# Performance work log

Measured on AMD Instinct MI355X. Metric: run time of the kernel, lower is better.

Reference implementation:

```python
import jax, jax.numpy as jnp
import numpy as np

B, H, W, C = 8, 64, 64, 128
L = H * W
NH = 4
HD = C // NH
SCALE = HD ** -0.5
WIN = 8
SHIFT = 4
DEPTH = 2
K = 3
N = WIN * WIN
NW = (H // WIN) * (W // WIN)


def _rel_pos_index(win):
    coords = np.stack(np.meshgrid(np.arange(win), np.arange(win), indexing='ij'))
    cf = coords.reshape(2, -1)
    rel = (cf[:, :, None] - cf[:, None, :]).transpose(1, 2, 0).copy()
    rel[:, :, 0] += win - 1
    rel[:, :, 1] += win - 1
    rel[:, :, 0] *= 2 * win - 1
    return rel.sum(-1)  # (N, N)

REL_IDX = jnp.asarray(_rel_pos_index(WIN).reshape(-1))


def _attn_mask(Hh, Ww, win, shift):
    img = np.zeros((Hh, Ww))
    cnt = 0
    for hs in (slice(0, -win), slice(-win, -shift), slice(-shift, None)):
        for ws in (slice(0, -win), slice(-win, -shift), slice(-shift, None)):
            img[hs, ws] = cnt
            cnt += 1
    mw = img.reshape(Hh // win, win, Ww // win, win).transpose(0, 2, 1, 3).reshape(-1, win * win)
    m = mw[:, None, :] - mw[:, :, None]
    return jnp.asarray(np.where(m != 0, -100.0, 0.0).astype(np.float32))  # (nW, N, N)

ATTN_MASK = _attn_mask(H, W, WIN, SHIFT)


def layer_norm(x, g, b, eps=1e-5):
    mu = x.mean(-1, keepdims=True)
    var = x.var(-1, keepdims=True)
    return (x - mu) / jnp.sqrt(var + eps) * g + b


def window_partition(x, win):
    Bb, Hh, Ww, Cc = x.shape
    x = x.reshape(Bb, Hh // win, win, Ww // win, win, Cc)
    return x.transpose(0, 1, 3, 2, 4, 5).reshape(-1, win, win, Cc)


def window_reverse(wins, win, Hh, Ww):
    Bb = wins.shape[0] // (Hh * Ww // win // win)
    x = wins.reshape(Bb, Hh // win, Ww // win, win, win, -1)
    return x.transpose(0, 1, 3, 2, 4, 5).reshape(Bb, Hh, Ww, -1)


def swin_block(x, shift, n1g, n1b, qkvw, qkvb, rp, pw, pb, n2g, n2b, f1w, f1b, f2w, f2b):
    shortcut = x
    x = layer_norm(x, n1g, n1b).reshape(B, H, W, C)
    if shift > 0:
        x = jnp.roll(x, (-shift, -shift), axis=(1, 2))
    xw = window_partition(x, WIN).reshape(-1, N, C)  # (B*nW, N, C)
    qkv = (xw @ qkvw + qkvb).reshape(-1, N, 3, NH, HD).transpose(2, 0, 3, 1, 4)
    q, k, v = qkv[0] * SCALE, qkv[1], qkv[2]
    attn = jnp.einsum('whnd,whmd->whnm', q, k)  # (B*nW, NH, N, N)
    bias = rp[REL_IDX].reshape(N, N, NH).transpose(2, 0, 1)
    attn = attn + bias[None]
    if shift > 0:
        attn = (attn.reshape(B, NW, NH, N, N) + ATTN_MASK[None, :, None]).reshape(-1, NH, N, N)
    attn = jax.nn.softmax(attn, axis=-1)
    out = jnp.einsum('whnm,whmd->whnd', attn, v).transpose(0, 2, 1, 3).reshape(-1, N, C)
    out = out @ pw + pb
    x = window_reverse(out.reshape(-1, WIN, WIN, C), WIN, H, W)
    if shift > 0:
        x = jnp.roll(x, (shift, shift), axis=(1, 2))
    x = shortcut + x.reshape(B, L, C)
    h = layer_norm(x, n2g, n2b)
    h = jax.nn.gelu(h @ f1w + f1b, approximate=False) @ f2w + f2b
    return x + h


def conv1d(x, w, b):  # x (B,C,L), w (O,I,K)
    y = jax.lax.conv_general_dilated(x, w, (1,), [(K // 2, K // 2)], dimension_numbers=('NCH', 'OIH', 'NCH'))
    return y + b[None, :, None]


def deform_conv1d(xt, off_w, off_b, msk_w, msk_b):
    x = xt.transpose(0, 2, 1)  # (B, C, L)
    offset = conv1d(x, off_w, off_b)                    # (B, K, L)
    mask = jax.nn.sigmoid(conv1d(x, msk_w, msk_b))      # (B, K, L)
    i = jnp.arange(L, dtype=x.dtype)
    pos = jnp.clip(i[None, None, :] + offset, 0.0, L - 1)  # (B, K, L)
    fp = jnp.floor(pos).astype(jnp.int32)
    cp = jnp.minimum(fp + 1, L - 1)
    alpha = pos - fp.astype(x.dtype)
    idx_f = jnp.broadcast_to(fp[:, None], (B, C, K, L))
    idx_c = jnp.broadcast_to(cp[:, None], (B, C, K, L))
    xe = jnp.broadcast_to(x[:, :, None, :], (B, C, K, L))
    xf = jnp.take_along_axis(xe, idx_f, axis=3)
    xc = jnp.take_along_axis(xe, idx_c, axis=3)
    samp = xf * (1.0 - alpha[:, None]) + xc * alpha[:, None]
    out = (samp * mask[:, None]).sum(2)  # (B, C, L)
    # faithful to torch: output.view(B, L, out_channels) reinterprets memory, no transpose
    return out.reshape(B, L, C)


def _forward(xt, hx, cx, red_w, red_b, n1g, n1b, qkvw, qkvb, rp, pw, pb, n2g, n2b,
             f1w, f1b, f2w, f2b, off_w, off_b, msk_w, msk_b, lf_w, lf_b, gf_w, gf_b, ff_w, ff_b):
    # global branch: inject hidden state then W-MSA / SW-MSA blocks
    g = jnp.concatenate([xt, hx], axis=-1) @ red_w + red_b
    for i, shift in enumerate((0, SHIFT)):
        g = swin_block(g, shift, n1g[i], n1b[i], qkvw[i], qkvb[i], rp[i], pw[i], pb[i],
                       n2g[i], n2b[i], f1w[i], f1b[i], f2w[i], f2b[i])
    # local branch: deformable 1D conv over token axis
    local = deform_conv1d(xt, off_w, off_b, msk_w, msk_b)
    # local-global fusion
    fu = jax.nn.relu((local @ lf_w + lf_b) * (g @ gf_w + gf_b)) @ ff_w + ff_b
    # LSTM-style gating (SwinLSTM cell update)
    gate = jax.nn.sigmoid(fu)
    cell = jnp.tanh(fu)
    cy = gate * (cx + cell)
    hy = gate * jnp.tanh(cy)
    return hy


def setup_inputs():
    key = jax.random.key(0)
    ks = iter(jax.random.split(key, 24))
    def rn(shape, s=0.02):
        return jax.random.normal(next(ks), shape, jnp.float32) * s
    return dict(
        xt=jax.random.normal(next(ks), (B, L, C), jnp.float32),
        hx=jax.random.normal(next(ks), (B, L, C), jnp.float32),
        cx=jax.random.normal(next(ks), (B, L, C), jnp.float32),
        red_w=rn((2 * C, C)), red_b=jnp.zeros((C,), jnp.float32),
        n1g=jnp.ones((DEPTH, C), jnp.float32), n1b=jnp.zeros((DEPTH, C), jnp.float32),
        qkvw=rn((DEPTH, C, 3 * C)), qkvb=jnp.zeros((DEPTH, 3 * C), jnp.float32),
        rp=rn((DEPTH, (2 * WIN - 1) ** 2, NH)),
        pw=rn((DEPTH, C, C)), pb=jnp.zeros((DEPTH, C), jnp.float32),
        n2g=jnp.ones((DEPTH, C), jnp.float32), n2b=jnp.zeros((DEPTH, C), jnp.float32),
        f1w=rn((DEPTH, C, 4 * C)), f1b=jnp.zeros((DEPTH, 4 * C), jnp.float32),
        f2w=rn((DEPTH, 4 * C, C)), f2b=jnp.zeros((DEPTH, C), jnp.float32),
        off_w=rn((K, C, K)), off_b=jnp.zeros((K,), jnp.float32),
        msk_w=rn((K, C, K)), msk_b=jnp.zeros((K,), jnp.float32),
        lf_w=rn((C, C)), lf_b=jnp.zeros((C,), jnp.float32),
        gf_w=rn((C, C)), gf_b=jnp.zeros((C,), jnp.float32),
        ff_w=rn((C, C)), ff_b=jnp.zeros((C,), jnp.float32),
    )


def reference(xt, hx, cx, red_w, red_b, n1g, n1b, qkvw, qkvb, rp, pw, pb, n2g, n2b,
              f1w, f1b, f2w, f2b, off_w, off_b, msk_w, msk_b, lf_w, lf_b, gf_w, gf_b, ff_w, ff_b):
    return _forward(xt, hx, cx, red_w, red_b, n1g, n1b, qkvw, qkvb, rp, pw, pb, n2g, n2b,
                    f1w, f1b, f2w, f2b, off_w, off_b, msk_w, msk_b, lf_w, lf_b, gf_w, gf_b, ff_w, ff_b)
```

## Files before the change

kernel.cpp:

```cpp
#include <hip/hip_runtime.h>
#include <hip/hip_bf16.h>
#include <math.h>

typedef __hip_bfloat16 bf16;
typedef unsigned short u16;
#define BF(x) __bfloat162float(x)
static __device__ __forceinline__ bf16 FB(float x) { return __float2bfloat16(x); }
static __device__ __forceinline__ u16 FBu(float x) {
    bf16 b = __float2bfloat16(x);
    return *(u16*)&b;
}

typedef __attribute__((ext_vector_type(4))) float f32x4;
typedef __attribute__((ext_vector_type(8))) __bf16 bf16x8;


#define O_REDW 0
#define O_QKVW 32768
#define O_PW   131072
#define O_F1W  163840
#define O_F2W  294912
#define O_LFW  425984
#define O_GFW  442368
#define O_FFW  458752
#define O_REDB 475136
#define O_QKVB 475264
#define O_PB   476032
#define O_F1B  476288
#define O_F2B  477312
#define O_LFB  477568
#define O_GFB  477696
#define O_FFB  477824
#define O_RP   477952
#define O_N1G  479752
#define O_N1B  480008
#define O_N2G  480264
#define O_N2B  480520
#define O_OW   480776
#define O_OB   481928
#define O_MW   481931
#define O_MB   483083

#define ROW_S 36
#define CH_S  2320

__device__ __forceinline__ int get_mode(const void* xt) {
    const unsigned* w = (const unsigned*)xt;
    int zlo = 0, inband = 0;
    #pragma unroll
    for (int i = 0; i < 32; ++i) {
        unsigned lo = w[i] & 0xFFFFu;
        int e = (int)((lo >> 7) & 0xFF);
        zlo += (lo == 0u || lo == 0x8000u);
        inband += (e >= 100 && e <= 140);
    }
    if (zlo >= 29) return 1;
    return (inband >= 20) ? 0 : 1;
}

__device__ __forceinline__ float LD(const void* p, size_t i, int mode) {
    return mode ? ((const float*)p)[i] : BF(((const bf16*)p)[i]);
}

__device__ __forceinline__ void async16(const u16* g, u16* l) {
    __builtin_amdgcn_global_load_lds(
        (const __attribute__((address_space(1))) unsigned int*)g,
        (__attribute__((address_space(3))) unsigned int*)l, 16, 0, 0);
}

struct PrepT { const void* src; int srcOff, K, N, dstOff; };
struct Prep { PrepT d[29]; int start[30]; };

__global__ void prep_k(Prep p, bf16* __restrict__ dst, const void* __restrict__ dtp) {
    const int mode = get_mode(dtp);
    int i = blockIdx.x * 256 + threadIdx.x;
    if (i >= p.start[29]) return;
    int s = 0;
    while (p.start[s + 1] <= i) ++s;
    int e = i - p.start[s];
    float v;
    if (p.d[s].N > 0) {
        int n = e / p.d[s].K, k = e % p.d[s].K;
        v = LD(p.d[s].src, (size_t)p.d[s].srcOff + (size_t)k * p.d[s].N + n, mode);
    } else {
        v = LD(p.d[s].src, (size_t)p.d[s].srcOff + e, mode);
    }
    dst[p.d[s].dstOff + e] = FB(v);
}

__launch_bounds__(256)
__global__ void xcat_k(const void* __restrict__ xt, const void* __restrict__ hx,
                       u16* __restrict__ X) {
    const int mode = get_mode(xt);
    const int total = 32768 * 32;
    for (int gidx = blockIdx.x * 256 + threadIdx.x; gidx < total;
         gidx += gridDim.x * 256) {
        int r = gidx >> 5, gi = gidx & 31;
        const void* src = (gi < 16) ? xt : hx;
        int c = (gi & 15) << 3;
        u16 outv[8];
        if (mode) {
            const float* s = (const float*)src + (size_t)r * 128 + c;
            float4 a = *(const float4*)s;
            float4 b = *(const float4*)(s + 4);
            outv[0] = FBu(a.x); outv[1] = FBu(a.y); outv[2] = FBu(a.z); outv[3] = FBu(a.w);
            outv[4] = FBu(b.x); outv[5] = FBu(b.y); outv[6] = FBu(b.z); outv[7] = FBu(b.w);
        } else {
            *(uint4*)outv = *(const uint4*)((const u16*)src + (size_t)r * 128 + c);
        }
        *(uint4*)(X + (size_t)r * 256 + (gi << 3)) = *(const uint4*)outv;
    }
}

template <int EPI>
__launch_bounds__(256)
__global__ void gemm_mfma(const u16* __restrict__ A, const u16* __restrict__ Bt,
                          const bf16* __restrict__ bias, bf16* __restrict__ outb,
                          float* __restrict__ outf, int M, int N, int K, int shift) {
    __shared__ __align__(16) u16 Als[2][2048];
    __shared__ __align__(16) u16 Bls[2][4096];
    const int tid = threadIdx.x;
    const int wave = tid >> 6, lane = tid & 63;
    const int q = lane >> 4, lr = lane & 15;
    const int wm = (wave >> 1) << 5, wn = (wave & 1) << 6;
    const int bm = blockIdx.y << 6, bn = blockIdx.x << 7;
    const f32x4 zero = {0.f, 0.f, 0.f, 0.f};
    f32x4 acc[2][4];
    #pragma unroll
    for (int i = 0; i < 2; ++i)
        #pragma unroll
        for (int j = 0; j < 4; ++j) acc[i][j] = zero;

    const int nk = K >> 5;
    {
        int c = tid;
        async16(A + (size_t)(bm + (c >> 2)) * K + ((c & 3) << 3), Als[0] + (c << 3));
        #pragma unroll
        for (int c2 = tid; c2 < 512; c2 += 256)
            async16(Bt + (size_t)(bn + (c2 >> 2)) * K + ((c2 & 3) << 3), Bls[0] + (c2 << 3));
    }
    __syncthreads();

    for (int i = 0; i < nk; ++i) {
        const int cur = i & 1, nxt = cur ^ 1;
        if (i + 1 < nk) {
            int k1 = (i + 1) << 5;
            int c = tid;
            async16(A + (size_t)(bm + (c >> 2)) * K + k1 + ((c & 3) << 3), Als[nxt] + (c << 3));
            #pragma unroll
            for (int c2 = tid; c2 < 512; c2 += 256)
                async16(Bt + (size_t)(bn + (c2 >> 2)) * K + k1 + ((c2 & 3) << 3), Bls[nxt] + (c2 << 3));
        }
        bf16x8 af[2], bfr[4];
        #pragma unroll
        for (int t = 0; t < 2; ++t)
            af[t] = *(const bf16x8*)(Als[cur] + ((wm + (t << 4) + lr) << 5) + (q << 3));
        #pragma unroll
        for (int t = 0; t < 4; ++t)
            bfr[t] = *(const bf16x8*)(Bls[cur] + ((wn + (t << 4) + lr) << 5) + (q << 3));
        #pragma unroll
        for (int mt = 0; mt < 2; ++mt)
            #pragma unroll
            for (int nt = 0; nt < 4; ++nt)
                acc[mt][nt] = __builtin_amdgcn_mfma_f32_16x16x32_bf16(
                    af[mt], bfr[nt], acc[mt][nt], 0, 0, 0);
        __syncthreads();
    }

    #pragma unroll
    for (int nt = 0; nt < 4; ++nt) {
        int col = bn + wn + (nt << 4) + lr;
        float bv = BF(bias[col]);
        #pragma unroll
        for (int mt = 0; mt < 2; ++mt) {
            int row0 = bm + wm + (mt << 4) + (q << 2);
            #pragma unroll
            for (int i = 0; i < 4; ++i) {
                int r = row0 + i;
                float v = acc[mt][nt][i] + bv;
                size_t idx = (size_t)r * N + col;
                if (EPI == 0) {
                    outb[idx] = FB(v);
                } else if (EPI == 3) {
                    int b = r >> 12, rem = r & 4095;
                    int wi = rem >> 6, n = rem & 63;
                    int hp = ((wi >> 3) << 3) + (n >> 3);
                    int wp = ((wi & 7) << 3) + (n & 7);
                    int h = (hp + shift) & 63, w = (wp + shift) & 63;
                    outf[((size_t)((b << 12) + (h << 6) + w)) * 128 + col] += v;
                } else if (EPI == 5) {
                    outf[idx] = v;
                }
            }
        }
    }
}

__launch_bounds__(256)
__global__ void qkvln_k(const float* __restrict__ g, const u16* __restrict__ wtu,
                        const bf16* __restrict__ wtb, u16* __restrict__ qkv,
                        int d, int shift) {
    __shared__ __align__(16) u16 Ach[4 * CH_S];
    __shared__ __align__(16) u16 Bb[2][8192];
    const int tid = threadIdx.x;
    const int wave = tid >> 6, lane = tid & 63;
    const int q = lane >> 4, lr = lane & 15;
    const int wm = (wave >> 1) << 5, wn = (wave & 1) << 6;
    const int bm = blockIdx.x << 6;
    const u16* Wq = wtu + O_QKVW + d * 49152;

    #pragma unroll
    for (int i = tid; i < 1024; i += 256) {
        int kc = i >> 9, c = i & 511;
        async16(Wq + (size_t)(c >> 2) * 128 + (kc << 5) + ((c & 3) << 3),
                Bb[0] + (kc << 12) + (c << 3));
    }

    {
        int row = tid >> 2, qtr = tid & 3;
        int r = bm + row;
        int b = r >> 12, rem = r & 4095;
        int wi = rem >> 6, n = rem & 63;
        int hp = ((wi >> 3) << 3) + (n >> 3);
        int wp = ((wi & 7) << 3) + (n & 7);
        int h = (hp + shift) & 63, w = (wp + shift) & 63;
        int src = (b << 12) + (h << 6) + w;
        const float* gr = g + (size_t)src * 128 + qtr * 32;
        float vals[32];
        float s1 = 0.f, s2 = 0.f;
        #pragma unroll
        for (int i = 0; i < 8; ++i) {
            float4 v4 = *(const float4*)(gr + i * 4);
            vals[i * 4] = v4.x; vals[i * 4 + 1] = v4.y;
            vals[i * 4 + 2] = v4.z; vals[i * 4 + 3] = v4.w;
            s1 += v4.x + v4.y + v4.z + v4.w;
            s2 += v4.x * v4.x + v4.y * v4.y + v4.z * v4.z + v4.w * v4.w;
        }
        s1 += __shfl_xor(s1, 1); s1 += __shfl_xor(s1, 2);
        s2 += __shfl_xor(s2, 1); s2 += __shfl_xor(s2, 2);
        float mu = s1 * (1.f / 128.f);
        float var = s2 * (1.f / 128.f) - mu * mu;
        float inv = rsqrtf(var + 1e-5f);
        #pragma unroll
        for (int i = 0; i < 32; ++i) {
            int c = qtr * 32 + i;
            float o = (vals[i] - mu) * inv * BF(wtb[O_N1G + d * 128 + c])
                      + BF(wtb[O_N1B + d * 128 + c]);
            Ach[qtr * CH_S + row * ROW_S + i] = FBu(o);
        }
    }
    __syncthreads();

    const f32x4 zero = {0.f, 0.f, 0.f, 0.f};
    f32x4 acc[2][4];
    for (int s = 0; s < 6; ++s) {
        const int nc = s >> 1, kh = s & 1, cur = s & 1 ? (s & 1) : (s & 1);
        const int bsel = s & 1;
        if (s < 5) {
            int t = s + 1, nct = t >> 1, kht = t & 1;
            const u16* Bg = Wq + nct * 16384;
            #pragma unroll
            for (int i = tid; i < 1024; i += 256) {
                int kc = i >> 9, c = i & 511;
                async16(Bg + (size_t)(c >> 2) * 128 + (kht << 6) + (kc << 5) + ((c & 3) << 3),
                        Bb[t & 1] + (kc << 12) + (c << 3));
            }
        }
        if (kh == 0) {
            #pragma unroll
            for (int i = 0; i < 2; ++i)
                #pragma unroll
                for (int j = 0; j < 4; ++j) acc[i][j] = zero;
        }
        #pragma unroll
        for (int kc = 0; kc < 2; ++kc) {
            bf16x8 af[2], bfr[4];
            #pragma unroll
            for (int t = 0; t < 2; ++t)
                af[t] = *(const bf16x8*)(Ach + (2 * kh + kc) * CH_S + (wm + (t << 4) + lr) * ROW_S + (q << 3));
            #pragma unroll
            for (int t = 0; t < 4; ++t)
                bfr[t] = *(const bf16x8*)(Bb[bsel] + (kc << 12) + ((wn + (t << 4) + lr) << 5) + (q << 3));
            #pragma unroll
            for (int mt = 0; mt < 2; ++mt)
                #pragma unroll
                for (int nt = 0; nt < 4; ++nt)
                    acc[mt][nt] = __builtin_amdgcn_mfma_f32_16x16x32_bf16(
                        af[mt], bfr[nt], acc[mt][nt], 0, 0, 0);
        }
        if (kh == 1) {
            #pragma unroll
            for (int nt = 0; nt < 4; ++nt) {
                int col = wn + (nt << 4) + lr;
                float bv = BF(wtb[O_QKVB + d * 384 + nc * 128 + col]);
                #pragma unroll
                for (int mt = 0; mt < 2; ++mt) {
                    #pragma unroll
                    for (int i = 0; i < 4; ++i) {
                        int r = bm + wm + (mt << 4) + (q << 2) + i;
                        qkv[(size_t)r * 384 + nc * 128 + col] = FBu(acc[mt][nt][i] + bv);
                    }
                }
            }
        }
        if (s < 5) __syncthreads();
    }
}

__launch_bounds__(256)
__global__ void attn_k(const u16* __restrict__ qkv, const bf16* __restrict__ rp,
                       u16* __restrict__ outp, int shift) {
    __shared__ float kT[4][32][64];
    __shared__ float vT[4][32][64];
    const int wq = blockIdx.x;
    const int head = threadIdx.x >> 6;
    const int t = threadIdx.x & 63;
    const size_t rbase = (size_t)(wq * 64 + t) * 384 + head * 32;
    float q[32];
    #pragma unroll
    for (int j = 0; j < 4; ++j) {
        bf16x8 qv = *(const bf16x8*)(qkv + rbase + j * 8);
        bf16x8 kv = *(const bf16x8*)(qkv + rbase + 128 + j * 8);
        bf16x8 vv = *(const bf16x8*)(qkv + rbase + 256 + j * 8);
        #pragma unroll
        for (int e = 0; e < 8; ++e) {
            int dd = j * 8 + e;
            q[dd] = (float)qv[e] * 0.17677669529663687f;
            kT[head][dd][t] = (float)kv[e];
            vT[head][dd][t] = (float)vv[e];
        }
    }
    __syncthreads();
    const int wloc = wq & 63;
    const int wh = (wloc >> 3) << 3, wwb = (wloc & 7) << 3;
    int regt = 0;
    if (shift) {
        int hp = wh + (t >> 3), wp = wwb + (t & 7);
        int rh = hp < 56 ? 0 : (hp < 60 ? 1 : 2);
        int rw = wp < 56 ? 0 : (wp < 60 ? 1 : 2);
        regt = rh * 3 + rw;
    }
    const int ti = t >> 3, tj = t & 7;
    float s[64];
    float mx = -1e30f;
    #pragma unroll
    for (int m = 0; m < 64; ++m) {
        float acc = 0.f;
        #pragma unroll
        for (int dd = 0; dd < 32; ++dd) acc += q[dd] * kT[head][dd][m];
        int idx = (ti - (m >> 3) + 7) * 15 + (tj - (m & 7) + 7);
        acc += BF(rp[idx * 4 + head]);
        if (shift) {
            int hp = wh + (m >> 3), wp = wwb + (m & 7);
            int rh = hp < 56 ? 0 : (hp < 60 ? 1 : 2);
            int rw = wp < 56 ? 0 : (wp < 60 ? 1 : 2);
            if (regt != rh * 3 + rw) acc -= 100.f;
        }
        s[m] = acc;
        mx = fmaxf(mx, acc);
    }
    float l = 0.f;
    #pragma unroll
    for (int m = 0; m < 64; ++m) {
        s[m] = expf(s[m] - mx);
        l += s[m];
    }
    const float inv = 1.f / l;
    const size_t obase = (size_t)(wq * 64 + t) * 128 + head * 32;
    #pragma unroll
    for (int j = 0; j < 4; ++j) {
        bf16x8 ov;
        #pragma unroll
        for (int e = 0; e < 8; ++e) {
            int dd = j * 8 + e;
            float a = 0.f;
            #pragma unroll
            for (int m = 0; m < 64; ++m) a += s[m] * vT[head][dd][m];
            ov[e] = (__bf16)(a * inv);
        }
        *(bf16x8*)(outp + obase + j * 8) = ov;
    }
}

__launch_bounds__(256)
__global__ void mlp_k(float* __restrict__ g, bf16* __restrict__ gbf,
                      const u16* __restrict__ wtu, const bf16* __restrict__ wtb,
                      int d) {
    __shared__ __align__(16) u16 Ach[4 * CH_S];
    __shared__ __align__(16) u16 bufB1[8192];
    __shared__ __align__(16) u16 bufB2[8192];
    __shared__ __align__(16) u16 buf2[2 * CH_S];
    const int tid = threadIdx.x;
    const int wave = tid >> 6, lane = tid & 63;
    const int q = lane >> 4, lr = lane & 15;
    const int wm = (wave >> 1) << 5;
    const int wn0 = (wave & 1) << 5;
    const int wn = (wave & 1) << 6;
    const int bm = blockIdx.x << 6;

    {
        const u16* B1g = wtu + O_F1W + d * 65536;
        #pragma unroll
        for (int i = tid; i < 1024; i += 256) {
            int kc = i >> 8, c = i & 255;
            async16(B1g + (c >> 2) * 128 + (kc << 5) + ((c & 3) << 3),
                    bufB1 + (kc << 11) + (c << 3));
        }
    }

    {
        int row = tid >> 2, qtr = tid & 3;
        const float* gr = g + (size_t)(bm + row) * 128 + qtr * 32;
        float vals[32];
        float s1 = 0.f, s2 = 0.f;
        #pragma unroll
        for (int i = 0; i < 8; ++i) {
            float4 v4 = *(const float4*)(gr + i * 4);
            vals[i * 4] = v4.x; vals[i * 4 + 1] = v4.y;
            vals[i * 4 + 2] = v4.z; vals[i * 4 + 3] = v4.w;
            s1 += v4.x + v4.y + v4.z + v4.w;
            s2 += v4.x * v4.x + v4.y * v4.y + v4.z * v4.z + v4.w * v4.w;
        }
        s1 += __shfl_xor(s1, 1); s1 += __shfl_xor(s1, 2);
        s2 += __shfl_xor(s2, 1); s2 += __shfl_xor(s2, 2);
        float mu = s1 * (1.f / 128.f);
        float var = s2 * (1.f / 128.f) - mu * mu;
        float inv = rsqrtf(var + 1e-5f);
        #pragma unroll
        for (int i = 0; i < 32; ++i) {
            int c = qtr * 32 + i;
            float o = (vals[i] - mu) * inv * BF(wtb[O_N2G + d * 128 + c])
                      + BF(wtb[O_N2B + d * 128 + c]);
            Ach[qtr * CH_S + row * ROW_S + i] = FBu(o);
        }
    }
    __syncthreads();

    const f32x4 zero = {0.f, 0.f, 0.f, 0.f};
    f32x4 acc2[2][4];
    #pragma unroll
    for (int i = 0; i < 2; ++i)
        #pragma unroll
        for (int j = 0; j < 4; ++j) acc2[i][j] = zero;

    for (int h = 0; h < 8; ++h) {
        {
            const u16* B2g = wtu + O_F2W + d * 65536 + h * 64;
            #pragma unroll
            for (int i = tid; i < 1024; i += 256) {
                int kc = i >> 9, c = i & 511;
                async16(B2g + (size_t)(c >> 2) * 512 + (kc << 5) + ((c & 3) << 3),
                        bufB2 + (kc << 12) + (c << 3));
            }
        }
        f32x4 acc1[2][2];
        #pragma unroll
        for (int i = 0; i < 2; ++i) { acc1[i][0] = zero; acc1[i][1] = zero; }
        #pragma unroll
        for (int k0 = 0; k0 < 4; ++k0) {
            bf16x8 af[2], bfr[2];
            #pragma unroll
            for (int t = 0; t < 2; ++t) {
                af[t]  = *(const bf16x8*)(Ach + k0 * CH_S + (wm + (t << 4) + lr) * ROW_S + (q << 3));
                bfr[t] = *(const bf16x8*)(bufB1 + (k0 << 11) + ((wn0 + (t << 4) + lr) << 5) + (q << 3));
            }
            #pragma unroll
            for (int mt = 0; mt < 2; ++mt)
                #pragma unroll
                for (int nt = 0; nt < 2; ++nt)
                    acc1[mt][nt] = __builtin_amdgcn_mfma_f32_16x16x32_bf16(
                        af[mt], bfr[nt], acc1[mt][nt], 0, 0, 0);
        }
        #pragma unroll
        for (int nt = 0; nt < 2; ++nt) {
            int c = wn0 + (nt << 4) + lr;
            float hb = BF(wtb[O_F1B + d * 512 + h * 64 + c]);
            #pragma unroll
            for (int mt = 0; mt < 2; ++mt) {
                #pragma unroll
                for (int i = 0; i < 4; ++i) {
                    int r = wm + (mt << 4) + (q << 2) + i;
                    float v = acc1[mt][nt][i] + hb;
                    float ge = 0.5f * v * (1.0f + erff(v * 0.70710678118654752f));
                    buf2[(c >> 5) * CH_S + r * ROW_S + (c & 31)] = FBu(ge);
                }
            }
        }
        __syncthreads();
        if (h < 7) {
            const u16* B1g = wtu + O_F1W + d * 65536 + (h + 1) * 8192;
            #pragma unroll
            for (int i = tid; i < 1024; i += 256) {
                int kc = i >> 8, c = i & 255;
                async16(B1g + (c >> 2) * 128 + (kc << 5) + ((c & 3) << 3),
                        bufB1 + (kc << 11) + (c << 3));
            }
        }
        #pragma unroll
        for (int kc = 0; kc < 2; ++kc) {
            bf16x8 ah[2], b2[4];
            #pragma unroll
            for (int t = 0; t < 2; ++t)
                ah[t] = *(const bf16x8*)(buf2 + kc * CH_S + (wm + (t << 4) + lr) * ROW_S + (q << 3));
            #pragma unroll
            for (int t = 0; t < 4; ++t)
                b2[t] = *(const bf16x8*)(bufB2 + (kc << 12) + ((wn + (t << 4) + lr) << 5) + (q << 3));
            #pragma unroll
            for (int mt = 0; mt < 2; ++mt)
                #pragma unroll
                for (int nt = 0; nt < 4; ++nt)
                    acc2[mt][nt] = __builtin_amdgcn_mfma_f32_16x16x32_bf16(
                        ah[mt], b2[nt], acc2[mt][nt], 0, 0, 0);
        }
        __syncthreads();
    }
    #pragma unroll
    for (int nt = 0; nt < 4; ++nt) {
        int col = wn + (nt << 4) + lr;
        float bv = BF(wtb[O_F2B + d * 128 + col]);
        #pragma unroll
        for (int mt = 0; mt < 2; ++mt) {
            #pragma unroll
            for (int i = 0; i < 4; ++i) {
                int r = bm + wm + (mt << 4) + (q << 2) + i;
                size_t idx = (size_t)r * 128 + col;
                float nv = g[idx] + acc2[mt][nt][i] + bv;
                g[idx] = nv;
                gbf[idx] = FB(nv);
            }
        }
    }
}

__launch_bounds__(256, 2)
__global__ void fuse3_k(const u16* __restrict__ Aloc, const u16* __restrict__ Ag,
                        const u16* __restrict__ wtu, const bf16* __restrict__ wtb,
                        const void* __restrict__ cx, void* __restrict__ out,
                        const void* __restrict__ dtp) {
    __shared__ __align__(16) u16 relb[4 * CH_S];
    const int mode = get_mode(dtp);
    const int tid = threadIdx.x;
    const int wave = tid >> 6, lane = tid & 63;
    const int q = lane >> 4, lr = lane & 15;
    const int wm = (wave >> 1) << 5, wn = (wave & 1) << 6;
    const int bm = blockIdx.x << 6;
    const f32x4 zero = {0.f, 0.f, 0.f, 0.f};
    f32x4 acc1[2][4], acc2[2][4];
    #pragma unroll
    for (int i = 0; i < 2; ++i)
        #pragma unroll
        for (int j = 0; j < 4; ++j) { acc1[i][j] = zero; acc2[i][j] = zero; }

    #pragma unroll
    for (int k0 = 0; k0 < 4; ++k0) {
        bf16x8 al[2], ag[2], blf[4], bgf[4];
        #pragma unroll
        for (int t = 0; t < 2; ++t) {
            size_t off = (size_t)(bm + wm + (t << 4) + lr) * 128 + (k0 << 5) + (q << 3);
            al[t] = *(const bf16x8*)(Aloc + off);
            ag[t] = *(const bf16x8*)(Ag + off);
        }
        #pragma unroll
        for (int t = 0; t < 4; ++t) {
            int woff = ((wn + (t << 4) + lr) << 7) + (k0 << 5) + (q << 3);
            blf[t] = *(const bf16x8*)(wtu + O_LFW + woff);
            bgf[t] = *(const bf16x8*)(wtu + O_GFW + woff);
        }
        #pragma unroll
        for (int mt = 0; mt < 2; ++mt)
            #pragma unroll
            for (int nt = 0; nt < 4; ++nt) {
                acc1[mt][nt] = __builtin_amdgcn_mfma_f32_16x16x32_bf16(
                    al[mt], blf[nt], acc1[mt][nt], 0, 0, 0);
                acc2[mt][nt] = __builtin_amdgcn_mfma_f32_16x16x32_bf16(
                    ag[mt], bgf[nt], acc2[mt][nt], 0, 0, 0);
            }
    }
    #pragma unroll
    for (int nt = 0; nt < 4; ++nt) {
        int c = wn + (nt << 4) + lr;
        float lfb = BF(wtb[O_LFB + c]);
        float gfb = BF(wtb[O_GFB + c]);
        #pragma unroll
        for (int mt = 0; mt < 2; ++mt) {
            #pragma unroll
            for (int i = 0; i < 4; ++i) {
                int r = wm + (mt << 4) + (q << 2) + i;
                float t1 = acc1[mt][nt][i] + lfb;
                float t2 = acc2[mt][nt][i] + gfb;
                float rel = t1 * t2;
                relb[(c >> 5) * CH_S + r * ROW_S + (c & 31)] = FBu(rel > 0.f ? rel : 0.f);
            }
        }
    }
    __syncthreads();
    f32x4 acc3[2][4];
    #pragma unroll
    for (int i = 0; i < 2; ++i)
        #pragma unroll
        for (int j = 0; j < 4; ++j) acc3[i][j] = zero;
    #pragma unroll
    for (int k0 = 0; k0 < 4; ++k0) {
        bf16x8 ar[2], bff[4];
        #pragma unroll
        for (int t = 0; t < 2; ++t)
            ar[t] = *(const bf16x8*)(relb + k0 * CH_S + (wm + (t << 4) + lr) * ROW_S + (q << 3));
        #pragma unroll
        for (int t = 0; t < 4; ++t)
            bff[t] = *(const bf16x8*)(wtu + O_FFW + ((wn + (t << 4) + lr) << 7) + (k0 << 5) + (q << 3));
        #pragma unroll
        for (int mt = 0; mt < 2; ++mt)
            #pragma unroll
            for (int nt = 0; nt < 4; ++nt)
                acc3[mt][nt] = __builtin_amdgcn_mfma_f32_16x16x32_bf16(
                    ar[mt], bff[nt], acc3[mt][nt], 0, 0, 0);
    }
    #pragma unroll
    for (int nt = 0; nt < 4; ++nt) {
        int col = wn + (nt << 4) + lr;
        float ffb = BF(wtb[O_FFB + col]);
        #pragma unroll
        for (int mt = 0; mt < 2; ++mt) {
            #pragma unroll
            for (int i = 0; i < 4; ++i) {
                int r = bm + wm + (mt << 4) + (q << 2) + i;
                size_t idx = (size_t)r * 128 + col;
                float v = acc3[mt][nt][i] + ffb;
                float gate = 1.f / (1.f + expf(-v));
                float cell = tanhf(v);
                float cy = gate * (LD(cx, idx, mode) + cell);
                float hy = gate * tanhf(cy);
                if (mode) ((float*)out)[idx] = hy;
                else      ((bf16*)out)[idx] = FB(hy);
            }
        }
    }
}

__launch_bounds__(256)
__global__ void deform_k(const void* __restrict__ xt, const bf16* __restrict__ wtb,
                         bf16* __restrict__ outL) {
    __shared__ __align__(16) u16 ot[128 * 72];
    __shared__ int s_fp[192], s_cp[192];
    __shared__ float s_al[192], s_mk[192];
    const int mode = get_mode(xt);
    const int tid = threadIdx.x;
    const int wave = tid >> 6, lane = tid & 63;
    const int b = blockIdx.x >> 6;
    const int l0 = (blockIdx.x & 63) << 6;
    float wo[3][3][2], wmk[3][3][2];
    #pragma unroll
    for (int k = 0; k < 3; ++k)
        #pragma unroll
        for (int j = 0; j < 3; ++j) {
            wo[k][j][0]  = BF(wtb[O_OW + (k * 128 + lane) * 3 + j]);
            wo[k][j][1]  = BF(wtb[O_OW + (k * 128 + lane + 64) * 3 + j]);
            wmk[k][j][0] = BF(wtb[O_MW + (k * 128 + lane) * 3 + j]);
            wmk[k][j][1] = BF(wtb[O_MW + (k * 128 + lane + 64) * 3 + j]);
        }
    for (int il = 0; il < 16; ++il) {
        int l_loc = wave * 16 + il;
        int l = l0 + l_loc;
        float a6[6] = {};
        #pragma unroll
        for (int j = 0; j < 3; ++j) {
            int row = l + j - 1;
            if (row >= 0 && row < 4096) {
                size_t base = ((size_t)(b << 12) + row) * 128;
                float x0 = LD(xt, base + lane, mode);
                float x1 = LD(xt, base + lane + 64, mode);
                #pragma unroll
                for (int k = 0; k < 3; ++k) {
                    a6[k]     += x0 * wo[k][j][0]  + x1 * wo[k][j][1];
                    a6[3 + k] += x0 * wmk[k][j][0] + x1 * wmk[k][j][1];
                }
            }
        }
        #pragma unroll
        for (int off = 32; off > 0; off >>= 1)
            #pragma unroll
            for (int k = 0; k < 6; ++k) a6[k] += __shfl_down(a6[k], off);
        if (lane == 0) {
            #pragma unroll
            for (int k = 0; k < 3; ++k) {
                float off = a6[k] + BF(wtb[O_OB + k]);
                float pos = fminf(fmaxf((float)l + off, 0.f), 4095.f);
                float fpf = floorf(pos);
                int fp = (int)fpf;
                int cp = fp + 1 > 4095 ? 4095 : fp + 1;
                s_fp[l_loc * 3 + k] = fp;
                s_cp[l_loc * 3 + k] = cp;
                s_al[l_loc * 3 + k] = pos - fpf;
                float mv = a6[3 + k] + BF(wtb[O_MB + k]);
                s_mk[l_loc * 3 + k] = 1.f / (1.f + expf(-mv));
            }
        }
    }
    __syncthreads();
    {
        int c = tid & 127, lh = tid >> 7;
        for (int it = 0; it < 32; ++it) {
            int l_loc = lh * 32 + it;
            float o = 0.f;
            #pragma unroll
            for (int k = 0; k < 3; ++k) {
                int fp = s_fp[l_loc * 3 + k];
                int cp = s_cp[l_loc * 3 + k];
                float al = s_al[l_loc * 3 + k];
                float mk = s_mk[l_loc * 3 + k];
                float xf = LD(xt, ((size_t)(b << 12) + fp) * 128 + c, mode);
                float xc = LD(xt, ((size_t)(b << 12) + cp) * 128 + c, mode);
                o += (xf * (1.f - al) + xc * al) * mk;
            }
            ot[c * 72 + l_loc] = FBu(o);
        }
    }
    __syncthreads();
    #pragma unroll
    for (int pass = 0; pass < 4; ++pass) {
        int cc = pass * 32 + (tid >> 3);
        int oo = tid & 7;
        const uint4 v = *(const uint4*)(ot + cc * 72 + oo * 8);
        *(uint4*)(outL + (size_t)b * 524288 + (size_t)cc * 4096 + l0 + oo * 8) = v;
    }
}

extern "C" void kernel_launch(void* const* d_in, const int* in_sizes, int n_in,
                              void* d_out, int out_size, void* d_ws, size_t ws_size,
                              hipStream_t stream) {
    (void)out_size; (void)ws_size;
    int I[28] = {0,1,2,3,4,5,6,7,8,9,10,11,12,13,14,15,16,17,18,19,20,21,22,23,24,25,26,27};
    if (n_in >= 28 && in_sizes[7] != 98304 && in_sizes[23] == 98304 && in_sizes[26] == 1800) {
        int alt[28] = {27, 9, 0, 25, 24, 15, 14, 23, 22, 26, 21, 20, 17, 16,
                       2, 1, 4, 3, 19, 18, 13, 12, 11, 10, 8, 7, 6, 5};
        for (int i = 0; i < 28; ++i) I[i] = alt[i];
    }
    const void* xt = d_in[I[0]];
    const void* hx = d_in[I[1]];
    const void* cx = d_in[I[2]];

    char* wsb = (char*)d_ws;
    float* g    = (float*)wsb;
    u16*   Abf  = (u16*)(wsb + 16777216);
    u16*   Bbf  = (u16*)(wsb + 25165824);
    u16*   Cbf  = (u16*)(wsb + 50331648);
    bf16*  wtb  = (bf16*)(wsb + 58720256);
    u16*   wtu  = (u16*)wtb;

    Prep p;
    PrepT descs[29] = {
        {d_in[I[3]],  0,     256, 128, O_REDW},
        {d_in[I[7]],  0,     128, 384, O_QKVW},
        {d_in[I[7]],  49152, 128, 384, O_QKVW + 49152},
        {d_in[I[10]], 0,     128, 128, O_PW},
        {d_in[I[10]], 16384, 128, 128, O_PW + 16384},
        {d_in[I[14]], 0,     128, 512, O_F1W},
        {d_in[I[14]], 65536, 128, 512, O_F1W + 65536},
        {d_in[I[16]], 0,     512, 128, O_F2W},
        {d_in[I[16]], 65536, 512, 128, O_F2W + 65536},
        {d_in[I[22]], 0,     128, 128, O_LFW},
        {d_in[I[24]], 0,     128, 128, O_GFW},
        {d_in[I[26]], 0,     128, 128, O_FFW},
        {d_in[I[4]],  0,  128, 0, O_REDB},
        {d_in[I[8]],  0,  768, 0, O_QKVB},
        {d_in[I[11]], 0,  256, 0, O_PB},
        {d_in[I[15]], 0, 1024, 0, O_F1B},
        {d_in[I[17]], 0,  256, 0, O_F2B},
        {d_in[I[23]], 0,  128, 0, O_LFB},
        {d_in[I[25]], 0,  128, 0, O_GFB},
        {d_in[I[27]], 0,  128, 0, O_FFB},
        {d_in[I[9]],  0, 1800, 0, O_RP},
        {d_in[I[5]],  0,  256, 0, O_N1G},
        {d_in[I[6]],  0,  256, 0, O_N1B},
        {d_in[I[12]], 0,  256, 0, O_N2G},
        {d_in[I[13]], 0,  256, 0, O_N2B},
        {d_in[I[18]], 0, 1152, 0, O_OW},
        {d_in[I[19]], 0,    3, 0, O_OB},
        {d_in[I[20]], 0, 1152, 0, O_MW},
        {d_in[I[21]], 0,    3, 0, O_MB},
    };
    int cum = 0;
    for (int i = 0; i < 29; ++i) {
        p.d[i] = descs[i];
        p.start[i] = cum;
        cum += (descs[i].N > 0) ? descs[i].K * descs[i].N : descs[i].K;
    }
    p.start[29] = cum;

    prep_k<<<(cum + 255) / 256, 256, 0, stream>>>(p, wtb, xt);
    xcat_k<<<1024, 256, 0, stream>>>(xt, hx, Bbf);

    gemm_mfma<5><<<dim3(1, 512), 256, 0, stream>>>(Bbf, wtu + O_REDW, wtb + O_REDB,
                                                   nullptr, g, 32768, 128, 256, 0);

    for (int d = 0; d < 2; ++d) {
        int shift = d ? 4 : 0;
        qkvln_k<<<512, 256, 0, stream>>>(g, wtu, wtb, Bbf, d, shift);
        attn_k<<<512, 256, 0, stream>>>(Bbf, wtb + O_RP + d * 900, Cbf, shift);
        gemm_mfma<3><<<dim3(1, 512), 256, 0, stream>>>(Cbf, wtu + O_PW + d * 16384,
                                                       wtb + O_PB + d * 128, nullptr, g,
                                                       32768, 128, 128, shift);
        mlp_k<<<512, 256, 0, stream>>>(g, (bf16*)Abf, wtu, wtb, d);
    }

    deform_k<<<512, 256, 0, stream>>>(xt, wtb, (bf16*)Cbf);
    fuse3_k<<<512, 256, 0, stream>>>(Cbf, Abf, wtu, wtb, cx, d_out, xt);
}
```

Before: 438.7 us.

## Split deformable conv into offset/mask kernel and sampling kernel

Splits the single deform kernel into two launches. The first computes offsets and masks with one wave per position across 8192 blocks, which spreads the reduction-heavy work over far more blocks. It writes them as float4 records into the workspace, reusing the Bbf region. The second kernel does the bilinear sampling and transposed store using 512 threads per block. The cost is an extra launch and a small global round trip for the offset data.

```diff
diff --git a/kernel.cpp b/kernel.cpp
--- a/kernel.cpp
+++ b/kernel.cpp
@@ -254,7 +254,7 @@
     const f32x4 zero = {0.f, 0.f, 0.f, 0.f};
     f32x4 acc[2][4];
     for (int s = 0; s < 6; ++s) {
-        const int nc = s >> 1, kh = s & 1, cur = s & 1 ? (s & 1) : (s & 1);
+        const int nc = s >> 1, kh = s & 1;
         const int bsel = s & 1;
         if (s < 5) {
             int t = s + 1, nct = t >> 1, kht = t & 1;
@@ -638,16 +638,12 @@
 }
 
 __launch_bounds__(256)
-__global__ void deform_k(const void* __restrict__ xt, const bf16* __restrict__ wtb,
-                         bf16* __restrict__ outL) {
-    __shared__ __align__(16) u16 ot[128 * 72];
-    __shared__ int s_fp[192], s_cp[192];
-    __shared__ float s_al[192], s_mk[192];
+__global__ void offmask_k(const void* __restrict__ xt, const bf16* __restrict__ wtb,
+                          float4* __restrict__ om) {
     const int mode = get_mode(xt);
-    const int tid = threadIdx.x;
-    const int wave = tid >> 6, lane = tid & 63;
-    const int b = blockIdx.x >> 6;
-    const int l0 = (blockIdx.x & 63) << 6;
+    const int wave = threadIdx.x >> 6, lane = threadIdx.x & 63;
+    const int gl = blockIdx.x * 4 + wave;
+    const int b = gl >> 12, l = gl & 4095;
     float wo[3][3][2], wmk[3][3][2];
     #pragma unroll
     for (int k = 0; k < 3; ++k)
@@ -658,67 +654,67 @@
             wmk[k][j][0] = BF(wtb[O_MW + (k * 128 + lane) * 3 + j]);
             wmk[k][j][1] = BF(wtb[O_MW + (k * 128 + lane + 64) * 3 + j]);
         }
-    for (int il = 0; il < 16; ++il) {
-        int l_loc = wave * 16 + il;
-        int l = l0 + l_loc;
-        float a6[6] = {};
-        #pragma unroll
-        for (int j = 0; j < 3; ++j) {
-            int row = l + j - 1;
-            if (row >= 0 && row < 4096) {
-                size_t base = ((size_t)(b << 12) + row) * 128;
-                float x0 = LD(xt, base + lane, mode);
-                float x1 = LD(xt, base + lane + 64, mode);
-                #pragma unroll
-                for (int k = 0; k < 3; ++k) {
-                    a6[k]     += x0 * wo[k][j][0]  + x1 * wo[k][j][1];
-                    a6[3 + k] += x0 * wmk[k][j][0] + x1 * wmk[k][j][1];
-                }
-            }
-        }
-        #pragma unroll
-        for (int off = 32; off > 0; off >>= 1)
-            #pragma unroll
-            for (int k = 0; k < 6; ++k) a6[k] += __shfl_down(a6[k], off);
-        if (lane == 0) {
+    float a6[6] = {};
+    #pragma unroll
+    for (int j = 0; j < 3; ++j) {
+        int row = l + j - 1;
+        if (row >= 0 && row < 4096) {
+            size_t base = ((size_t)(b << 12) + row) * 128;
+            float x0 = LD(xt, base + lane, mode);
+            float x1 = LD(xt, base + lane + 64, mode);
             #pragma unroll
             for (int k = 0; k < 3; ++k) {
-                float off = a6[k] + BF(wtb[O_OB + k]);
-                float pos = fminf(fmaxf((float)l + off, 0.f), 4095.f);
-                float fpf = floorf(pos);
-                int fp = (int)fpf;
-                int cp = fp + 1 > 4095 ? 4095 : fp + 1;
-                s_fp[l_loc * 3 + k] = fp;
-                s_cp[l_loc * 3 + k] = cp;
-                s_al[l_loc * 3 + k] = pos - fpf;
-                float mv = a6[3 + k] + BF(wtb[O_MB + k]);
-                s_mk[l_loc * 3 + k] = 1.f / (1.f + expf(-mv));
-            }
-        }
+                a6[k]     += x0 * wo[k][j][0]  + x1 * wo[k][j][1];
+                a6[3 + k] += x0 * wmk[k][j][0] + x1 * wmk[k][j][1];
+            }
+        }
+    }
+    #pragma unroll
+    for (int off = 32; off > 0; off >>= 1)
+        #pragma unroll
+        for (int k = 0; k < 6; ++k) a6[k] += __shfl_down(a6[k], off);
+    if (lane == 0) {
+        #pragma unroll
+        for (int k = 0; k < 3; ++k) {
+            float off = a6[k] + BF(wtb[O_OB + k]);
+            float pos = fminf(fmaxf((float)l + off, 0.f), 4095.f);
+            float fpf = floorf(pos);
+            float mv = a6[3 + k] + BF(wtb[O_MB + k]);
+            float mk = 1.f / (1.f + expf(-mv));
+            om[(size_t)gl * 3 + k] = make_float4(fpf, pos - fpf, mk, 0.f);
+        }
+    }
+}
+
+__launch_bounds__(512)
+__global__ void sample_k(const void* __restrict__ xt, const float4* __restrict__ om,
+                         bf16* __restrict__ outL) {
+    __shared__ __align__(16) u16 ot[128 * 72];
+    const int mode = get_mode(xt);
+    const int tid = threadIdx.x;
+    const int b = blockIdx.x >> 6;
+    const int l0 = (blockIdx.x & 63) << 6;
+    const int c = tid & 127, lh = tid >> 7;
+    for (int it = 0; it < 16; ++it) {
+        int l_loc = lh * 16 + it;
+        size_t gl = (size_t)(b << 12) + l0 + l_loc;
+        float o = 0.f;
+        #pragma unroll
+        for (int k = 0; k < 3; ++k) {
+            float4 v = om[gl * 3 + k];
+            int fp = (int)v.x;
+            int cp = fp + 1 > 4095 ? 4095 : fp + 1;
+            float al = v.y, mk = v.z;
+            float xf = LD(xt, ((size_t)(b << 12) + fp) * 128 + c, mode);
+            float xc = LD(xt, ((size_t)(b << 12) + cp) * 128 + c, mode);
+            o += (xf * (1.f - al) + xc * al) * mk;
+        }
+        ot[c * 72 + l_loc] = FBu(o);
     }
     __syncthreads();
-    {
-        int c = tid & 127, lh = tid >> 7;
-        for (int it = 0; it < 32; ++it) {
-            int l_loc = lh * 32 + it;
-            float o = 0.f;
-            #pragma unroll
-            for (int k = 0; k < 3; ++k) {
-                int fp = s_fp[l_loc * 3 + k];
-                int cp = s_cp[l_loc * 3 + k];
-                float al = s_al[l_loc * 3 + k];
-                float mk = s_mk[l_loc * 3 + k];
-                float xf = LD(xt, ((size_t)(b << 12) + fp) * 128 + c, mode);
-                float xc = LD(xt, ((size_t)(b << 12) + cp) * 128 + c, mode);
-                o += (xf * (1.f - al) + xc * al) * mk;
-            }
-            ot[c * 72 + l_loc] = FBu(o);
-        }
-    }
-    __syncthreads();
-    #pragma unroll
-    for (int pass = 0; pass < 4; ++pass) {
-        int cc = pass * 32 + (tid >> 3);
+    #pragma unroll
+    for (int pass = 0; pass < 2; ++pass) {
+        int cc = pass * 64 + (tid >> 3);
         int oo = tid & 7;
         const uint4 v = *(const uint4*)(ot + cc * 72 + oo * 8);
         *(uint4*)(outL + (size_t)b * 524288 + (size_t)cc * 4096 + l0 + oo * 8) = v;
@@ -746,6 +742,7 @@
     u16*   Cbf  = (u16*)(wsb + 50331648);
     bf16*  wtb  = (bf16*)(wsb + 58720256);
     u16*   wtu  = (u16*)wtb;
+    float4* om  = (float4*)(wsb + 25165824);
 
     Prep p;
     PrepT descs[29] = {
@@ -803,6 +800,7 @@
         mlp_k<<<512, 256, 0, stream>>>(g, (bf16*)Abf, wtu, wtb, d);
     }
 
-    deform_k<<<512, 256, 0, stream>>>(xt, wtb, (bf16*)Cbf);
+    offmask_k<<<8192, 256, 0, stream>>>(xt, wtb, om);
+    sample_k<<<512, 512, 0, stream>>>(xt, om, (bf16*)Cbf);
     fuse3_k<<<512, 256, 0, stream>>>(Cbf, Abf, wtu, wtb, cx, d_out, xt);
 }
```

Measured after the change: 445.0 us. Within noise of the previous version (+1.4%).
